# Kernel tuning notes

Hardware: AMD Instinct MI355X
Metric: run time of the kernel (lower is better)

Reference implementation:

```python
import jax, jax.numpy as jnp
import numpy as np

N_ETYPES = 6
N_STEPS = 5
N_ITERS = 6
N_LSTM_LAYERS = 3
NODES_PER_GRAPH = 200


def _uinit(key, shape, fan_in):
    s = 1.0 / np.sqrt(fan_in)
    return jax.random.uniform(key, shape, jnp.float32, -s, s)


def setup_inputs() -> dict:
    key = jax.random.key(0)
    ks = jax.random.split(key, 24)
    N, D = 64000, 64
    G = N // NODES_PER_GRAPH  # 320 graphs
    E = N * 16  # 1,024,000 edges
    feats = jax.random.normal(ks[0], (N, D), jnp.float32)
    # within-graph edges: local endpoint + graph offset
    graph_of_edge = jnp.repeat(jnp.arange(G, dtype=jnp.int32), E // G)
    src = jax.random.randint(ks[1], (E,), 0, NODES_PER_GRAPH, jnp.int32) + graph_of_edge * NODES_PER_GRAPH
    dst = jax.random.randint(ks[2], (E,), 0, NODES_PER_GRAPH, jnp.int32) + graph_of_edge * NODES_PER_GRAPH
    etypes = jax.random.randint(ks[3], (E,), 0, N_ETYPES, jnp.int32)
    node_graph = jnp.repeat(jnp.arange(G, dtype=jnp.int32), NODES_PER_GRAPH)
    # GatedGraphConv params: per-etype Linear(D,D) + GRUCell(D,D) (torch gate order r,z,n)
    W_edge = _uinit(ks[4], (N_ETYPES, D, D), D)
    b_edge = _uinit(ks[5], (N_ETYPES, D), D)
    gru_W_ih = _uinit(ks[6], (3 * D, D), D)
    gru_W_hh = _uinit(ks[7], (3 * D, D), D)
    gru_b_ih = _uinit(ks[8], (3 * D,), D)
    gru_b_hh = _uinit(ks[9], (3 * D,), D)
    # Set2Set LSTM: 3 layers, input 2D (layer0) / D (layers 1,2), hidden D; torch gate order i,f,g,o
    lstm_W_ih0 = _uinit(ks[10], (4 * D, 2 * D), D)
    lstm_W_hh0 = _uinit(ks[11], (4 * D, D), D)
    lstm_b_ih0 = _uinit(ks[12], (4 * D,), D)
    lstm_b_hh0 = _uinit(ks[13], (4 * D,), D)
    lstm_W_ih1 = _uinit(ks[14], (4 * D, D), D)
    lstm_W_hh1 = _uinit(ks[15], (4 * D, D), D)
    lstm_b_ih1 = _uinit(ks[16], (4 * D,), D)
    lstm_b_hh1 = _uinit(ks[17], (4 * D,), D)
    lstm_W_ih2 = _uinit(ks[18], (4 * D, D), D)
    lstm_W_hh2 = _uinit(ks[19], (4 * D, D), D)
    lstm_b_ih2 = _uinit(ks[20], (4 * D,), D)
    lstm_b_hh2 = _uinit(ks[21], (4 * D,), D)
    Wp = _uinit(ks[22], (3, 2 * D), 2 * D)
    bp = _uinit(ks[23], (3,), 2 * D)
    return dict(feats=feats, W_edge=W_edge, b_edge=b_edge,
                gru_W_ih=gru_W_ih, gru_W_hh=gru_W_hh, gru_b_ih=gru_b_ih, gru_b_hh=gru_b_hh,
                lstm_W_ih0=lstm_W_ih0, lstm_W_hh0=lstm_W_hh0, lstm_b_ih0=lstm_b_ih0, lstm_b_hh0=lstm_b_hh0,
                lstm_W_ih1=lstm_W_ih1, lstm_W_hh1=lstm_W_hh1, lstm_b_ih1=lstm_b_ih1, lstm_b_hh1=lstm_b_hh1,
                lstm_W_ih2=lstm_W_ih2, lstm_W_hh2=lstm_W_hh2, lstm_b_ih2=lstm_b_ih2, lstm_b_hh2=lstm_b_hh2,
                Wp=Wp, bp=bp, src=src, dst=dst, etypes=etypes, node_graph=node_graph)


def _ggnn_forward(feats, W_edge, b_edge, gru_W_ih, gru_W_hh, gru_b_ih, gru_b_hh,
                  lstm_params, Wp, bp, src, dst, etypes, node_graph):
    N, D = feats.shape
    G = N // NODES_PER_GRAPH
    h = feats
    # --- GatedGraphConv: 5 steps of etype-typed transform + scatter-sum + GRU ---
    for _ in range(N_STEPS):
        # transform every node by every etype weight (cheap: N << E), then gather per edge
        Wh = jnp.einsum('nd,tdo->tno', h, W_edge) + b_edge[:, None, :]  # [T,N,D]
        msg = Wh[etypes, src]                                           # [E,D] gather
        a = jax.ops.segment_sum(msg, dst, num_segments=N)               # [N,D] scatter-add
        gi = a @ gru_W_ih.T + gru_b_ih
        gh = h @ gru_W_hh.T + gru_b_hh
        i_r, i_z, i_n = jnp.split(gi, 3, -1)
        h_r, h_z, h_n = jnp.split(gh, 3, -1)
        r = jax.nn.sigmoid(i_r + h_r)
        z = jax.nn.sigmoid(i_z + h_z)
        n = jnp.tanh(i_n + r * h_n)
        h = (1.0 - z) * n + z * h
    feat = h
    # --- Set2Set readout ---
    q_star = jnp.zeros((G, 2 * D), feat.dtype)
    hs = jnp.zeros((N_LSTM_LAYERS, G, D), feat.dtype)
    cs = jnp.zeros((N_LSTM_LAYERS, G, D), feat.dtype)
    for _ in range(N_ITERS):
        x = q_star
        new_h, new_c = [], []
        for l, (Wi, Whh, bi, bh) in enumerate(lstm_params):
            gates = x @ Wi.T + bi + hs[l] @ Whh.T + bh
            ii, ff, gg, oo = jnp.split(gates, 4, -1)
            c = jax.nn.sigmoid(ff) * cs[l] + jax.nn.sigmoid(ii) * jnp.tanh(gg)
            x = jax.nn.sigmoid(oo) * jnp.tanh(c)
            new_h.append(x)
            new_c.append(c)
        hs = jnp.stack(new_h)
        cs = jnp.stack(new_c)
        q = x  # [G,D]
        e = jnp.sum(feat * q[node_graph], axis=-1)                         # [N]
        emax = jax.ops.segment_max(e, node_graph, num_segments=G)
        ex = jnp.exp(e - emax[node_graph])
        denom = jax.ops.segment_sum(ex, node_graph, num_segments=G)
        alpha = ex / denom[node_graph]                                     # segment softmax
        readout = jax.ops.segment_sum(feat * alpha[:, None], node_graph, num_segments=G)
        q_star = jnp.concatenate([q, readout], axis=-1)
    return q_star @ Wp.T + bp  # [G,3]


def reference(feats, W_edge, b_edge, gru_W_ih, gru_W_hh, gru_b_ih, gru_b_hh,
              lstm_W_ih0, lstm_W_hh0, lstm_b_ih0, lstm_b_hh0,
              lstm_W_ih1, lstm_W_hh1, lstm_b_ih1, lstm_b_hh1,
              lstm_W_ih2, lstm_W_hh2, lstm_b_ih2, lstm_b_hh2,
              Wp, bp, src, dst, etypes, node_graph):
    lstm_params = [
        (lstm_W_ih0, lstm_W_hh0, lstm_b_ih0, lstm_b_hh0),
        (lstm_W_ih1, lstm_W_hh1, lstm_b_ih1, lstm_b_hh1),
        (lstm_W_ih2, lstm_W_hh2, lstm_b_ih2, lstm_b_hh2),
    ]
    return _ggnn_forward(feats, W_edge, b_edge, gru_W_ih, gru_W_hh, gru_b_ih, gru_b_hh,
                         lstm_params, Wp, bp, src, dst, etypes, node_graph)
```

## Files before the change

kernel.cpp:

```cpp
#include <hip/hip_runtime.h>

typedef unsigned short u16;
typedef unsigned int u32;

#define DIM 64
#define NGRAPH 320
#define NPG 200
#define EPG 3200
#define NSTEPS 5
#define NITERS 6
#define NTILES 13
#define NPAD 208
#define NTHR 1024

typedef __attribute__((ext_vector_type(8))) short bf16x8;
typedef __attribute__((ext_vector_type(4))) float f32x4;

__device__ __forceinline__ float bf2f(u16 u) {
  u32 x = ((u32)u) << 16;
  float f;
  __builtin_memcpy(&f, &x, 4);
  return f;
}
__device__ __forceinline__ u16 f2bf(float f) {
  u32 x;
  __builtin_memcpy(&x, &f, 4);
  x = (x + 0x7FFFu + ((x >> 16) & 1u)) >> 16;
  return (u16)x;
}
__device__ __forceinline__ float bflo(u32 w) {
  u32 x = w << 16;
  float f;
  __builtin_memcpy(&f, &x, 4);
  return f;
}
__device__ __forceinline__ float bfhi(u32 w) {
  u32 x = w & 0xffff0000u;
  float f;
  __builtin_memcpy(&f, &x, 4);
  return f;
}
__device__ __forceinline__ float sigmf(float x) { return 1.0f / (1.0f + __expf(-x)); }
__device__ __forceinline__ int swz(int row, int col) { return row * 64 + (col ^ ((row & 7) << 3)); }


__global__ void __launch_bounds__(256) k_csr(const int* __restrict__ src,
                                             const int* __restrict__ dst,
                                             const int* __restrict__ ety,
                                             u16* __restrict__ recs,
                                             int* __restrict__ rows) {
  __shared__ int cnt[3 * NPG];
  __shared__ int rofs[3 * (NPG + 1)];
  int g = blockIdx.x, tid = threadIdx.x;
  int base = g * NPG;
  for (int i = tid; i < 3 * NPG; i += 256) cnt[i] = 0;
  __syncthreads();
  for (int e = tid; e < EPG; e += 256) {
    int d = dst[g * EPG + e] - base;
    int t = ety[g * EPG + e];
    atomicAdd(&cnt[(t >> 1) * NPG + d], 1);
  }
  __syncthreads();
  if (tid == 0) {
    int s = 0;
    for (int p = 0; p < 3; p++) {
      for (int n = 0; n < NPG; n++) {
        rofs[p * (NPG + 1) + n] = s;
        s += cnt[p * NPG + n];
      }
      rofs[p * (NPG + 1) + NPG] = s;
    }
  }
  __syncthreads();
  for (int i = tid; i < 3 * NPG; i += 256) cnt[i] = rofs[(i / NPG) * (NPG + 1) + (i % NPG)];
  __syncthreads();
  for (int e = tid; e < EPG; e += 256) {
    int d = dst[g * EPG + e] - base;
    int t = ety[g * EPG + e];
    int sl = src[g * EPG + e] - base;
    int pos = atomicAdd(&cnt[(t >> 1) * NPG + d], 1);
    recs[g * EPG + pos] = (u16)((t & 1) * NPG + sl);
  }
  for (int i = tid; i < 3 * (NPG + 1); i += 256) rows[g * 3 * (NPG + 1) + i] = rofs[i];
}

__global__ void __launch_bounds__(256) k_prep(
    const float* __restrict__ W_edge, const float* __restrict__ gWih, const float* __restrict__ gWhh,
    const float* __restrict__ lWi0, const float* __restrict__ lWh0,
    const float* __restrict__ lWi1, const float* __restrict__ lWh1,
    const float* __restrict__ lWi2, const float* __restrict__ lWh2,
    u16* __restrict__ WeTb, u16* __restrict__ Wihb, u16* __restrict__ Whhb,
    u16* __restrict__ WTih0b, u16* __restrict__ WThh0b,
    u16* __restrict__ WTih1b, u16* __restrict__ WThh1b,
    u16* __restrict__ WTih2b, u16* __restrict__ WThh2b) {
  int i = blockIdx.x * 256 + threadIdx.x;
  if (i < 24576) {
    int t = i >> 12, rem = i & 4095, o = rem >> 6, k = rem & 63;
    WeTb[i] = f2bf(W_edge[t * 4096 + k * 64 + o]);
  } else if (i < 36864) {
    int idx = i - 24576;
    Wihb[idx] = f2bf(gWih[idx]);
  } else if (i < 49152) {
    int idx = i - 36864;
    Whhb[idx] = f2bf(gWhh[idx]);
  } else if (i < 81920) {
    int idx = i - 49152;
    int k = idx >> 8, jj = idx & 255;
    WTih0b[idx] = f2bf(lWi0[jj * 128 + k]);
  } else {
    int idx = i - 81920;
    int seg = idx >> 14;
    int r = idx & 16383;
    int k = r >> 8, jj = r & 255;
    const float* sp = seg == 0 ? lWh0 : seg == 1 ? lWi1 : seg == 2 ? lWh1 : seg == 3 ? lWi2 : lWh2;
    u16* dp = seg == 0 ? WThh0b : seg == 1 ? WTih1b : seg == 2 ? WThh1b : seg == 3 ? WTih2b : WThh2b;
    dp[r] = f2bf(sp[jj * 64 + k]);
  }
}


__global__ void __launch_bounds__(NTHR, 4) k_ggnn(
    const float* __restrict__ feats,
    const u16* __restrict__ WeTb, const float* __restrict__ b_edge,
    const u16* __restrict__ Wihb, const u16* __restrict__ Whhb,
    const float* __restrict__ gbih, const float* __restrict__ gbhh,
    const u16* __restrict__ recs, const int* __restrict__ rows,
    const u16* __restrict__ WTih0b, const u16* __restrict__ WThh0b,
    const u16* __restrict__ WTih1b, const u16* __restrict__ WThh1b,
    const u16* __restrict__ WTih2b, const u16* __restrict__ WThh2b,
    const float* __restrict__ b_ih0, const float* __restrict__ b_hh0,
    const float* __restrict__ b_ih1, const float* __restrict__ b_hh1,
    const float* __restrict__ b_ih2, const float* __restrict__ b_hh2,
    const float* __restrict__ Wp, const float* __restrict__ bp,
    float* __restrict__ out) {
  __shared__ __align__(16) u16 hb_s[NPAD * 64];
  __shared__ __align__(16) u16 wh_s[2 * NPG * 64];
  __shared__ __align__(16) float acc_s[NPG * 64];
  __shared__ __align__(16) u16 rec_s[EPG];
  __shared__ int rows_s[3 * (NPG + 1)];
  __shared__ float qstar[128], xbuf[64], hs_s[3][64], cs_s[3][64];
  __shared__ float gates[256], gpart[4 * 256], e_s[NPG], red[16][64], scal[2];

  int g = blockIdx.x, tid = threadIdx.x;
  int lane = tid & 63, wid = tid >> 6;
  int m = lane & 15, quad = lane >> 4;
  int half = lane >> 5, l32 = lane & 31;

  const float* fg = feats + (size_t)g * (NPG * 64);
  for (int i = tid; i < NPG * 64; i += NTHR) hb_s[swz(i >> 6, i & 63)] = f2bf(fg[i]);
  for (int i = tid; i < (NPAD - NPG) * 64; i += NTHR) hb_s[NPG * 64 + i] = 0;
  {
    const u32* r32 = (const u32*)(recs + (size_t)g * EPG);
    u32* rl = (u32*)rec_s;
    for (int i = tid; i < EPG / 2; i += NTHR) rl[i] = r32[i];
  }
  for (int i = tid; i < 3 * (NPG + 1); i += NTHR) rows_s[i] = rows[g * 3 * (NPG + 1) + i];

  float hreg[4][4] = {};
  if (wid < NTILES) {
#pragma unroll
    for (int r = 0; r < 4; r++) {
      int node = wid * 16 + quad * 4 + r;
      if (node < NPG) {
#pragma unroll
        for (int dq = 0; dq < 4; dq++) hreg[r][dq] = fg[node * 64 + dq * 16 + m];
      }
    }
  }

  u16* ab_s = wh_s;
  int ot = wid & 3, hh = wid >> 2;

#pragma unroll 1
  for (int step = 0; step < NSTEPS; step++) {
    __syncthreads();
    {
      float4* z4 = (float4*)acc_s;
      float4 z = {0.f, 0.f, 0.f, 0.f};
      for (int i = tid; i < NPG * 16; i += NTHR) z4[i] = z;
    }
#pragma unroll 1
    for (int ph = 0; ph < 3; ph++) {
      if (ph > 0) __syncthreads();
      {
        const u16* bp0 = WeTb + (((2 * ph) * 64 + ot * 16 + m) * 64) + quad * 8;
        const u16* bp1 = WeTb + (((2 * ph + 1) * 64 + ot * 16 + m) * 64) + quad * 8;
        bf16x8 B00 = *(const bf16x8*)bp0;
        bf16x8 B01 = *(const bf16x8*)(bp0 + 32);
        bf16x8 B10 = *(const bf16x8*)bp1;
        bf16x8 B11 = *(const bf16x8*)(bp1 + 32);
        float bias0 = b_edge[(2 * ph) * 64 + ot * 16 + m];
        float bias1 = b_edge[(2 * ph + 1) * 64 + ot * 16 + m];
        for (int nt = hh; nt < NTILES; nt += 4) {
          int arow = nt * 16 + m;
          bf16x8 a0 = *(const bf16x8*)(hb_s + swz(arow, quad * 8));
          bf16x8 a1 = *(const bf16x8*)(hb_s + swz(arow, quad * 8 + 32));
          f32x4 c = {0.f, 0.f, 0.f, 0.f};
          c = __builtin_amdgcn_mfma_f32_16x16x32_bf16(a0, B00, c, 0, 0, 0);
          c = __builtin_amdgcn_mfma_f32_16x16x32_bf16(a1, B01, c, 0, 0, 0);
#pragma unroll
          for (int r = 0; r < 4; r++) {
            int node = nt * 16 + quad * 4 + r;
            if (node < NPG) wh_s[node * 64 + ot * 16 + m] = f2bf(c[r] + bias0);
          }
        }
        for (int nt = 3 - hh; nt < NTILES; nt += 4) {
          int arow = nt * 16 + m;
          bf16x8 a0 = *(const bf16x8*)(hb_s + swz(arow, quad * 8));
          bf16x8 a1 = *(const bf16x8*)(hb_s + swz(arow, quad * 8 + 32));
          f32x4 c = {0.f, 0.f, 0.f, 0.f};
          c = __builtin_amdgcn_mfma_f32_16x16x32_bf16(a0, B10, c, 0, 0, 0);
          c = __builtin_amdgcn_mfma_f32_16x16x32_bf16(a1, B11, c, 0, 0, 0);
#pragma unroll
          for (int r = 0; r < 4; r++) {
            int node = nt * 16 + quad * 4 + r;
            if (node < NPG) wh_s[(NPG + node) * 64 + ot * 16 + m] = f2bf(c[r] + bias1);
          }
        }
      }
      __syncthreads();
      const int* rowp = rows_s + ph * (NPG + 1);
      for (int q = 0; q < 13; q++) {
        int n = q * 16 + wid;
        if (n >= NPG) continue;
        int rs = rowp[n], re = rowp[n + 1];
        float r0 = 0.f, r1 = 0.f;
        int e = rs;
        for (; e + 4 <= re; e += 4) {
          int pA = rec_s[e + half];
          int pB = rec_s[e + 2 + half];
          u32 wA = *(const u32*)(wh_s + pA * 64 + 2 * l32);
          u32 wB = *(const u32*)(wh_s + pB * 64 + 2 * l32);
          r0 += bflo(wA) + bflo(wB);
          r1 += bfhi(wA) + bfhi(wB);
        }
        if (e + 2 <= re) {
          int pA = rec_s[e + half];
          u32 wA = *(const u32*)(wh_s + pA * 64 + 2 * l32);
          r0 += bflo(wA);
          r1 += bfhi(wA);
          e += 2;
        }
        if (e < re && half == 0) {
          int pA = rec_s[e];
          u32 wA = *(const u32*)(wh_s + pA * 64 + 2 * l32);
          r0 += bflo(wA);
          r1 += bfhi(wA);
        }
        r0 += __shfl_xor(r0, 32);
        r1 += __shfl_xor(r1, 32);
        if (lane < 32) {
          float2* p = (float2*)(acc_s + n * 64 + 2 * l32);
          float2 v = *p;
          v.x += r0;
          v.y += r1;
          *p = v;
        }
      }
    }
    __syncthreads();
    for (int idx = tid; idx < NPG * 32; idx += NTHR) {
      int n = idx >> 5, jj = idx & 31;
      float2 v = *(const float2*)(acc_s + n * 64 + 2 * jj);
      u32 pk = (u32)f2bf(v.x) | ((u32)f2bf(v.y) << 16);
      *(u32*)(ab_s + n * 64 + ((2 * jj) ^ ((n & 7) << 3))) = pk;
    }
    __syncthreads();
    if (wid < NTILES) {
      int nt = wid;
      int arow = nt * 16 + m;
      bf16x8 aa0 = *(const bf16x8*)(ab_s + swz(arow, quad * 8));
      bf16x8 aa1 = *(const bf16x8*)(ab_s + swz(arow, quad * 8 + 32));
      bf16x8 ah0 = *(const bf16x8*)(hb_s + swz(arow, quad * 8));
      bf16x8 ah1 = *(const bf16x8*)(hb_s + swz(arow, quad * 8 + 32));
#pragma unroll
      for (int dq = 0; dq < 4; dq++) {
        int d = dq * 16 + m;
        f32x4 z4 = {0.f, 0.f, 0.f, 0.f};
        const u16* bi = Wihb + (dq * 16 + m) * 64 + quad * 8;
        const u16* bh = Whhb + (dq * 16 + m) * 64 + quad * 8;
        f32x4 cr = z4;
        {
          bf16x8 b0 = *(const bf16x8*)bi, b1 = *(const bf16x8*)(bi + 32);
          bf16x8 c0 = *(const bf16x8*)bh, c1 = *(const bf16x8*)(bh + 32);
          cr = __builtin_amdgcn_mfma_f32_16x16x32_bf16(ah0, c0, cr, 0, 0, 0);
          cr = __builtin_amdgcn_mfma_f32_16x16x32_bf16(ah1, c1, cr, 0, 0, 0);
          cr = __builtin_amdgcn_mfma_f32_16x16x32_bf16(aa0, b0, cr, 0, 0, 0);
          cr = __builtin_amdgcn_mfma_f32_16x16x32_bf16(aa1, b1, cr, 0, 0, 0);
        }
        const u16* bi2 = Wihb + ((4 + dq) * 16 + m) * 64 + quad * 8;
        const u16* bh2 = Whhb + ((4 + dq) * 16 + m) * 64 + quad * 8;
        f32x4 cz = z4;
        {
          bf16x8 b0 = *(const bf16x8*)bi2, b1 = *(const bf16x8*)(bi2 + 32);
          bf16x8 c0 = *(const bf16x8*)bh2, c1 = *(const bf16x8*)(bh2 + 32);
          cz = __builtin_amdgcn_mfma_f32_16x16x32_bf16(ah0, c0, cz, 0, 0, 0);
          cz = __builtin_amdgcn_mfma_f32_16x16x32_bf16(ah1, c1, cz, 0, 0, 0);
          cz = __builtin_amdgcn_mfma_f32_16x16x32_bf16(aa0, b0, cz, 0, 0, 0);
          cz = __builtin_amdgcn_mfma_f32_16x16x32_bf16(aa1, b1, cz, 0, 0, 0);
        }
        const u16* bi3 = Wihb + ((8 + dq) * 16 + m) * 64 + quad * 8;
        const u16* bh3 = Whhb + ((8 + dq) * 16 + m) * 64 + quad * 8;
        f32x4 ci = z4, ch = z4;
        {
          bf16x8 b0 = *(const bf16x8*)bi3, b1 = *(const bf16x8*)(bi3 + 32);
          bf16x8 c0 = *(const bf16x8*)bh3, c1 = *(const bf16x8*)(bh3 + 32);
          ci = __builtin_amdgcn_mfma_f32_16x16x32_bf16(aa0, b0, ci, 0, 0, 0);
          ci = __builtin_amdgcn_mfma_f32_16x16x32_bf16(aa1, b1, ci, 0, 0, 0);
          ch = __builtin_amdgcn_mfma_f32_16x16x32_bf16(ah0, c0, ch, 0, 0, 0);
          ch = __builtin_amdgcn_mfma_f32_16x16x32_bf16(ah1, c1, ch, 0, 0, 0);
        }
        float bi_r = gbih[d], bh_r = gbhh[d];
        float bi_z = gbih[64 + d], bh_z = gbhh[64 + d];
        float bi_n = gbih[128 + d], bh_n = gbhh[128 + d];
#pragma unroll
        for (int r = 0; r < 4; r++) {
          int node = nt * 16 + quad * 4 + r;
          if (node < NPG) {
            float rr = sigmf(cr[r] + bi_r + bh_r);
            float zz = sigmf(cz[r] + bi_z + bh_z);
            float nn = tanhf(ci[r] + bi_n + rr * (ch[r] + bh_n));
            float hv = hreg[r][dq];
            float hnew = (1.0f - zz) * nn + zz * hv;
            hreg[r][dq] = hnew;
            hb_s[swz(node, d)] = f2bf(hnew);
            if (step == NSTEPS - 1) acc_s[node * 64 + d] = hnew;
          }
        }
      }
    }
  }
  __syncthreads();
  const float* feat_s = acc_s;

  int j = tid & 255, part = tid >> 8;
  float bs0 = 0.f, bs1 = 0.f, bs2 = 0.f;
  if (tid < 256) {
    bs0 = b_ih0[tid] + b_hh0[tid];
    bs1 = b_ih1[tid] + b_hh1[tid];
    bs2 = b_ih2[tid] + b_hh2[tid];
  }
  if (tid < 128) qstar[tid] = 0.f;
  if (tid < 64) {
    xbuf[tid] = 0.f;
    for (int l = 0; l < 3; l++) {
      hs_s[l][tid] = 0.f;
      cs_s[l][tid] = 0.f;
    }
  }
  __syncthreads();
#pragma unroll 1
  for (int it = 0; it < NITERS; it++) {
    {
      float a0 = 0.f;
      if (part == 0) {
#pragma unroll 8
        for (int k = 0; k < 48; k++) a0 += qstar[k] * bf2f(WTih0b[k * 256 + j]);
      } else if (part == 1) {
#pragma unroll 8
        for (int k = 48; k < 96; k++) a0 += qstar[k] * bf2f(WTih0b[k * 256 + j]);
      } else if (part == 2) {
#pragma unroll 8
        for (int k = 96; k < 128; k++) a0 += qstar[k] * bf2f(WTih0b[k * 256 + j]);
#pragma unroll 8
        for (int k = 0; k < 16; k++) a0 += hs_s[0][k] * bf2f(WThh0b[k * 256 + j]);
      } else {
#pragma unroll 8
        for (int k = 16; k < 64; k++) a0 += hs_s[0][k] * bf2f(WThh0b[k * 256 + j]);
      }
      gpart[part * 256 + j] = a0;
    }
    __syncthreads();
    if (tid < 256)
      gates[tid] = gpart[tid] + gpart[256 + tid] + gpart[512 + tid] + gpart[768 + tid] + bs0;
    __syncthreads();
    if (tid < 64) {
      float cc = sigmf(gates[64 + tid]) * cs_s[0][tid] + sigmf(gates[tid]) * tanhf(gates[128 + tid]);
      float x = sigmf(gates[192 + tid]) * tanhf(cc);
      cs_s[0][tid] = cc;
      hs_s[0][tid] = x;
      xbuf[tid] = x;
    }
    __syncthreads();
#pragma unroll 1
    for (int l = 1; l < 3; l++) {
      const u16* W = (l == 1) ? ((part < 2) ? WTih1b : WThh1b)
                              : ((part < 2) ? WTih2b : WThh2b);
      const float* xv = (part < 2) ? xbuf : hs_s[l];
      int k0 = (part & 1) * 32;
      float a0 = 0.f;
#pragma unroll 8
      for (int k = k0; k < k0 + 32; k++) a0 += xv[k] * bf2f(W[k * 256 + j]);
      gpart[part * 256 + j] = a0;
      __syncthreads();
      float bsl = (l == 1) ? bs1 : bs2;
      if (tid < 256)
        gates[tid] = gpart[tid] + gpart[256 + tid] + gpart[512 + tid] + gpart[768 + tid] + bsl;
      __syncthreads();
      if (tid < 64) {
        float cc = sigmf(gates[64 + tid]) * cs_s[l][tid] + sigmf(gates[tid]) * tanhf(gates[128 + tid]);
        float x = sigmf(gates[192 + tid]) * tanhf(cc);
        cs_s[l][tid] = cc;
        hs_s[l][tid] = x;
        xbuf[tid] = x;
      }
      __syncthreads();
    }
    for (int n = wid; n < NPG; n += 16) {
      float v = feat_s[n * 64 + lane] * xbuf[lane];
      for (int off = 32; off > 0; off >>= 1) v += __shfl_down(v, off);
      if (lane == 0) e_s[n] = v;
    }
    __syncthreads();
    if (tid < 64) {
      float mx = -1e30f;
      for (int n = lane; n < NPG; n += 64) mx = fmaxf(mx, e_s[n]);
      for (int off = 32; off > 0; off >>= 1) mx = fmaxf(mx, __shfl_down(mx, off));
      mx = __shfl(mx, 0);
      float ssum = 0.f;
      for (int n = lane; n < NPG; n += 64) {
        float ex = __expf(e_s[n] - mx);
        e_s[n] = ex;
        ssum += ex;
      }
      for (int off = 32; off > 0; off >>= 1) ssum += __shfl_down(ssum, off);
      if (lane == 0) scal[0] = ssum;
    }
    __syncthreads();
    float denom = scal[0];
    {
      float r = 0.f;
      for (int n = wid; n < NPG; n += 16) r += feat_s[n * 64 + lane] * e_s[n];
      red[wid][lane] = r;
    }
    __syncthreads();
    if (tid < 64) {
      float ro = 0.f;
#pragma unroll
      for (int ww = 0; ww < 16; ww++) ro += red[ww][lane];
      qstar[lane] = xbuf[lane];
      qstar[64 + lane] = ro / denom;
    }
    __syncthreads();
  }
  if (tid < 3) {
    float s = bp[tid];
    for (int k = 0; k < 128; k++) s += qstar[k] * Wp[tid * 128 + k];
    out[g * 3 + tid] = s;
  }
}


extern "C" void kernel_launch(void* const* d_in, const int* in_sizes, int n_in,
                              void* d_out, int out_size, void* d_ws, size_t ws_size,
                              hipStream_t stream) {
  const float* feats  = (const float*)d_in[0];
  const float* W_edge = (const float*)d_in[1];
  const float* b_edge = (const float*)d_in[2];
  const float* gWih   = (const float*)d_in[3];
  const float* gWhh   = (const float*)d_in[4];
  const float* gbih   = (const float*)d_in[5];
  const float* gbhh   = (const float*)d_in[6];
  const float* lWi0   = (const float*)d_in[7];
  const float* lWh0   = (const float*)d_in[8];
  const float* lbi0   = (const float*)d_in[9];
  const float* lbh0   = (const float*)d_in[10];
  const float* lWi1   = (const float*)d_in[11];
  const float* lWh1   = (const float*)d_in[12];
  const float* lbi1   = (const float*)d_in[13];
  const float* lbh1   = (const float*)d_in[14];
  const float* lWi2   = (const float*)d_in[15];
  const float* lWh2   = (const float*)d_in[16];
  const float* lbi2   = (const float*)d_in[17];
  const float* lbh2   = (const float*)d_in[18];
  const float* Wp     = (const float*)d_in[19];
  const float* bp     = (const float*)d_in[20];
  const int* src      = (const int*)d_in[21];
  const int* dst      = (const int*)d_in[22];
  const int* ety      = (const int*)d_in[23];
  float* out = (float*)d_out;

  char* ws = (char*)d_ws;
  u16* recs    = (u16*)ws;
  int* rows    = (int*)(ws + 2048000);
  u16* WeTb    = (u16*)(ws + 2819840);
  u16* Wihb    = (u16*)(ws + 2868992);
  u16* Whhb    = (u16*)(ws + 2893568);
  u16* WTih0b  = (u16*)(ws + 2918144);
  u16* WThh0b  = (u16*)(ws + 2983680);
  u16* WTih1b  = (u16*)(ws + 3016448);
  u16* WThh1b  = (u16*)(ws + 3049216);
  u16* WTih2b  = (u16*)(ws + 3081984);
  u16* WThh2b  = (u16*)(ws + 3114752);

  k_csr<<<NGRAPH, 256, 0, stream>>>(src, dst, ety, recs, rows);
  k_prep<<<640, 256, 0, stream>>>(W_edge, gWih, gWhh, lWi0, lWh0, lWi1, lWh1, lWi2, lWh2,
                                  WeTb, Wihb, Whhb, WTih0b, WThh0b, WTih1b, WThh1b, WTih2b, WThh2b);
  k_ggnn<<<NGRAPH, NTHR, 0, stream>>>(feats, WeTb, b_edge, Wihb, Whhb, gbih, gbhh, recs, rows,
                                      WTih0b, WThh0b, WTih1b, WThh1b, WTih2b, WThh2b,
                                      lbi0, lbh0, lbi1, lbh1, lbi2, lbh2, Wp, bp, out);
}
```

Baseline: 808.7 us.

## Halve block size, keep gather accumulators in registers, shrink shared memory

The fused GGNN kernel now runs 512 threads per graph instead of 1024. The edge CSR is split into six per-etype partitions so each message phase transforms only one etype into a single shared buffer. Per-node aggregation sums are held in 50 unrolled registers per thread rather than a float accumulator array in shared memory, and the final node features go to a global scratch buffer. The shared footprint shrinks and small buffers are aliased into one union, aiming for more resident blocks per CU and less LDS traffic, in exchange for more barriers per step (six phases instead of three), higher register pressure, and global reads during the Set2Set readout.

```diff
diff --git a/kernel.cpp b/kernel.cpp
--- a/kernel.cpp
+++ b/kernel.cpp
@@ -11,7 +11,7 @@
 #define NITERS 6
 #define NTILES 13
 #define NPAD 208
-#define NTHR 1024
+#define NTHR 512
 
 typedef __attribute__((ext_vector_type(8))) short bf16x8;
 typedef __attribute__((ext_vector_type(4))) float f32x4;
@@ -43,27 +43,30 @@
 __device__ __forceinline__ float sigmf(float x) { return 1.0f / (1.0f + __expf(-x)); }
 __device__ __forceinline__ int swz(int row, int col) { return row * 64 + (col ^ ((row & 7) << 3)); }
 
+#define REP25(M) M(0) M(1) M(2) M(3) M(4) M(5) M(6) M(7) M(8) M(9) M(10) M(11) M(12) \
+                 M(13) M(14) M(15) M(16) M(17) M(18) M(19) M(20) M(21) M(22) M(23) M(24)
+
 
 __global__ void __launch_bounds__(256) k_csr(const int* __restrict__ src,
                                              const int* __restrict__ dst,
                                              const int* __restrict__ ety,
                                              u16* __restrict__ recs,
                                              int* __restrict__ rows) {
-  __shared__ int cnt[3 * NPG];
-  __shared__ int rofs[3 * (NPG + 1)];
+  __shared__ int cnt[6 * NPG];
+  __shared__ int rofs[6 * (NPG + 1)];
   int g = blockIdx.x, tid = threadIdx.x;
   int base = g * NPG;
-  for (int i = tid; i < 3 * NPG; i += 256) cnt[i] = 0;
+  for (int i = tid; i < 6 * NPG; i += 256) cnt[i] = 0;
   __syncthreads();
   for (int e = tid; e < EPG; e += 256) {
     int d = dst[g * EPG + e] - base;
     int t = ety[g * EPG + e];
-    atomicAdd(&cnt[(t >> 1) * NPG + d], 1);
+    atomicAdd(&cnt[t * NPG + d], 1);
   }
   __syncthreads();
   if (tid == 0) {
     int s = 0;
-    for (int p = 0; p < 3; p++) {
+    for (int p = 0; p < 6; p++) {
       for (int n = 0; n < NPG; n++) {
         rofs[p * (NPG + 1) + n] = s;
         s += cnt[p * NPG + n];
@@ -72,16 +75,16 @@
     }
   }
   __syncthreads();
-  for (int i = tid; i < 3 * NPG; i += 256) cnt[i] = rofs[(i / NPG) * (NPG + 1) + (i % NPG)];
+  for (int i = tid; i < 6 * NPG; i += 256) cnt[i] = rofs[(i / NPG) * (NPG + 1) + (i % NPG)];
   __syncthreads();
   for (int e = tid; e < EPG; e += 256) {
     int d = dst[g * EPG + e] - base;
     int t = ety[g * EPG + e];
     int sl = src[g * EPG + e] - base;
-    int pos = atomicAdd(&cnt[(t >> 1) * NPG + d], 1);
-    recs[g * EPG + pos] = (u16)((t & 1) * NPG + sl);
-  }
-  for (int i = tid; i < 3 * (NPG + 1); i += 256) rows[g * 3 * (NPG + 1) + i] = rofs[i];
+    int pos = atomicAdd(&cnt[t * NPG + d], 1);
+    recs[g * EPG + pos] = (u16)sl;
+  }
+  for (int i = tid; i < 6 * (NPG + 1); i += 256) rows[g * 6 * (NPG + 1) + i] = rofs[i];
 }
 
 __global__ void __launch_bounds__(256) k_prep(
@@ -132,14 +135,22 @@
     const float* __restrict__ b_ih1, const float* __restrict__ b_hh1,
     const float* __restrict__ b_ih2, const float* __restrict__ b_hh2,
     const float* __restrict__ Wp, const float* __restrict__ bp,
-    float* __restrict__ out) {
+    float* __restrict__ featg, float* __restrict__ out) {
   __shared__ __align__(16) u16 hb_s[NPAD * 64];
-  __shared__ __align__(16) u16 wh_s[2 * NPG * 64];
-  __shared__ __align__(16) float acc_s[NPG * 64];
-  __shared__ __align__(16) u16 rec_s[EPG];
-  __shared__ int rows_s[3 * (NPG + 1)];
-  __shared__ float qstar[128], xbuf[64], hs_s[3][64], cs_s[3][64];
-  __shared__ float gates[256], gpart[4 * 256], e_s[NPG], red[16][64], scal[2];
+  __shared__ __align__(16) u16 whab[NPG * 64];
+  __shared__ __align__(16) char u_s[11232];
+
+  u16* rec_s = (u16*)u_s;
+  int* rows_s = (int*)(u_s + 6400);
+  float* qstar = (float*)u_s;
+  float* xbuf = (float*)(u_s + 512);
+  float* hs_f = (float*)(u_s + 768);
+  float* cs_f = (float*)(u_s + 1536);
+  float* gates = (float*)(u_s + 2304);
+  float* gpart = (float*)(u_s + 3328);
+  float* e_s = (float*)(u_s + 5376);
+  float* red_f = (float*)(u_s + 6176);
+  float* scal = (float*)(u_s + 8224);
 
   int g = blockIdx.x, tid = threadIdx.x;
   int lane = tid & 63, wid = tid >> 6;
@@ -147,6 +158,7 @@
   int half = lane >> 5, l32 = lane & 31;
 
   const float* fg = feats + (size_t)g * (NPG * 64);
+  float* fo = featg + (size_t)g * (NPG * 64);
   for (int i = tid; i < NPG * 64; i += NTHR) hb_s[swz(i >> 6, i & 63)] = f2bf(fg[i]);
   for (int i = tid; i < (NPAD - NPG) * 64; i += NTHR) hb_s[NPG * 64 + i] = 0;
   {
@@ -154,120 +166,107 @@
     u32* rl = (u32*)rec_s;
     for (int i = tid; i < EPG / 2; i += NTHR) rl[i] = r32[i];
   }
-  for (int i = tid; i < 3 * (NPG + 1); i += NTHR) rows_s[i] = rows[g * 3 * (NPG + 1) + i];
-
-  float hreg[4][4] = {};
-  if (wid < NTILES) {
-#pragma unroll
-    for (int r = 0; r < 4; r++) {
-      int node = wid * 16 + quad * 4 + r;
-      if (node < NPG) {
-#pragma unroll
-        for (int dq = 0; dq < 4; dq++) hreg[r][dq] = fg[node * 64 + dq * 16 + m];
-      }
-    }
-  }
-
-  u16* ab_s = wh_s;
-  int ot = wid & 3, hh = wid >> 2;
+  for (int i = tid; i < 6 * (NPG + 1); i += NTHR) rows_s[i] = rows[g * 6 * (NPG + 1) + i];
+
+  float hreg[2][4][4] = {};
+#pragma unroll
+  for (int ti = 0; ti < 2; ti++) {
+    int nt = wid + 8 * ti;
+    if (nt < NTILES) {
+#pragma unroll
+      for (int r = 0; r < 4; r++) {
+        int node = nt * 16 + quad * 4 + r;
+        if (node < NPG) {
+#pragma unroll
+          for (int dq = 0; dq < 4; dq++) hreg[ti][r][dq] = fg[node * 64 + dq * 16 + m];
+        }
+      }
+    }
+  }
+
+  u16* ab_s = whab;
+  int ot = wid & 3;
+
+#define ACC_DECL(q) float a0_##q, a1_##q;
+  REP25(ACC_DECL)
+#define ACC_ZERO(q) a0_##q = 0.f; a1_##q = 0.f;
+#define GATHER(q)                                                  \
+  {                                                                \
+    int n = (q)*8 + wid;                                           \
+    int rs = rowp[n], re = rowp[n + 1];                            \
+    float r0 = 0.f, r1 = 0.f;                                      \
+    int e = rs;                                                    \
+    for (; e + 4 <= re; e += 4) {                                  \
+      int pA = rec_s[e + half];                                    \
+      int pB = rec_s[e + 2 + half];                                \
+      u32 wA = *(const u32*)(whab + pA * 64 + 2 * l32);            \
+      u32 wB = *(const u32*)(whab + pB * 64 + 2 * l32);            \
+      r0 += bflo(wA) + bflo(wB);                                   \
+      r1 += bfhi(wA) + bfhi(wB);                                   \
+    }                                                              \
+    if (e + 2 <= re) {                                             \
+      int pA = rec_s[e + half];                                    \
+      u32 wA = *(const u32*)(whab + pA * 64 + 2 * l32);            \
+      r0 += bflo(wA);                                              \
+      r1 += bfhi(wA);                                              \
+      e += 2;                                                      \
+    }                                                              \
+    if (e < re && half == 0) {                                     \
+      int pA = rec_s[e];                                           \
+      u32 wA = *(const u32*)(whab + pA * 64 + 2 * l32);            \
+      r0 += bflo(wA);                                              \
+      r1 += bfhi(wA);                                              \
+    }                                                              \
+    a0_##q += r0;                                                  \
+    a1_##q += r1;                                                  \
+  }
+#define FLUSH(q)                                                   \
+  {                                                                \
+    float s0 = a0_##q + __shfl_xor(a0_##q, 32);                    \
+    float s1 = a1_##q + __shfl_xor(a1_##q, 32);                    \
+    if (lane < 32) {                                               \
+      int n = (q)*8 + wid;                                         \
+      u32 pk = (u32)f2bf(s0) | ((u32)f2bf(s1) << 16);              \
+      *(u32*)(ab_s + n * 64 + ((2 * l32) ^ ((n & 7) << 3))) = pk;  \
+    }                                                              \
+  }
 
 #pragma unroll 1
   for (int step = 0; step < NSTEPS; step++) {
-    __syncthreads();
-    {
-      float4* z4 = (float4*)acc_s;
-      float4 z = {0.f, 0.f, 0.f, 0.f};
-      for (int i = tid; i < NPG * 16; i += NTHR) z4[i] = z;
-    }
+    REP25(ACC_ZERO)
 #pragma unroll 1
-    for (int ph = 0; ph < 3; ph++) {
-      if (ph > 0) __syncthreads();
+    for (int t = 0; t < 6; t++) {
+      __syncthreads();
       {
-        const u16* bp0 = WeTb + (((2 * ph) * 64 + ot * 16 + m) * 64) + quad * 8;
-        const u16* bp1 = WeTb + (((2 * ph + 1) * 64 + ot * 16 + m) * 64) + quad * 8;
-        bf16x8 B00 = *(const bf16x8*)bp0;
-        bf16x8 B01 = *(const bf16x8*)(bp0 + 32);
-        bf16x8 B10 = *(const bf16x8*)bp1;
-        bf16x8 B11 = *(const bf16x8*)(bp1 + 32);
-        float bias0 = b_edge[(2 * ph) * 64 + ot * 16 + m];
-        float bias1 = b_edge[(2 * ph + 1) * 64 + ot * 16 + m];
-        for (int nt = hh; nt < NTILES; nt += 4) {
+        const u16* bpt = WeTb + ((t * 64 + ot * 16 + m) * 64) + quad * 8;
+        bf16x8 B0 = *(const bf16x8*)bpt;
+        bf16x8 B1 = *(const bf16x8*)(bpt + 32);
+        float bias = b_edge[t * 64 + ot * 16 + m];
+        for (int nt = (wid >> 2); nt < NTILES; nt += 2) {
           int arow = nt * 16 + m;
           bf16x8 a0 = *(const bf16x8*)(hb_s + swz(arow, quad * 8));
           bf16x8 a1 = *(const bf16x8*)(hb_s + swz(arow, quad * 8 + 32));
           f32x4 c = {0.f, 0.f, 0.f, 0.f};
-          c = __builtin_amdgcn_mfma_f32_16x16x32_bf16(a0, B00, c, 0, 0, 0);
-          c = __builtin_amdgcn_mfma_f32_16x16x32_bf16(a1, B01, c, 0, 0, 0);
+          c = __builtin_amdgcn_mfma_f32_16x16x32_bf16(a0, B0, c, 0, 0, 0);
+          c = __builtin_amdgcn_mfma_f32_16x16x32_bf16(a1, B1, c, 0, 0, 0);
 #pragma unroll
           for (int r = 0; r < 4; r++) {
             int node = nt * 16 + quad * 4 + r;
-            if (node < NPG) wh_s[node * 64 + ot * 16 + m] = f2bf(c[r] + bias0);
+            if (node < NPG) whab[node * 64 + ot * 16 + m] = f2bf(c[r] + bias);
           }
         }
-        for (int nt = 3 - hh; nt < NTILES; nt += 4) {
-          int arow = nt * 16 + m;
-          bf16x8 a0 = *(const bf16x8*)(hb_s + swz(arow, quad * 8));
-          bf16x8 a1 = *(const bf16x8*)(hb_s + swz(arow, quad * 8 + 32));
-          f32x4 c = {0.f, 0.f, 0.f, 0.f};
-          c = __builtin_amdgcn_mfma_f32_16x16x32_bf16(a0, B10, c, 0, 0, 0);
-          c = __builtin_amdgcn_mfma_f32_16x16x32_bf16(a1, B11, c, 0, 0, 0);
-#pragma unroll
-          for (int r = 0; r < 4; r++) {
-            int node = nt * 16 + quad * 4 + r;
-            if (node < NPG) wh_s[(NPG + node) * 64 + ot * 16 + m] = f2bf(c[r] + bias1);
-          }
-        }
       }
       __syncthreads();
-      const int* rowp = rows_s + ph * (NPG + 1);
-      for (int q = 0; q < 13; q++) {
-        int n = q * 16 + wid;
-        if (n >= NPG) continue;
-        int rs = rowp[n], re = rowp[n + 1];
-        float r0 = 0.f, r1 = 0.f;
-        int e = rs;
-        for (; e + 4 <= re; e += 4) {
-          int pA = rec_s[e + half];
-          int pB = rec_s[e + 2 + half];
-          u32 wA = *(const u32*)(wh_s + pA * 64 + 2 * l32);
-          u32 wB = *(const u32*)(wh_s + pB * 64 + 2 * l32);
-          r0 += bflo(wA) + bflo(wB);
-          r1 += bfhi(wA) + bfhi(wB);
-        }
-        if (e + 2 <= re) {
-          int pA = rec_s[e + half];
-          u32 wA = *(const u32*)(wh_s + pA * 64 + 2 * l32);
-          r0 += bflo(wA);
-          r1 += bfhi(wA);
-          e += 2;
-        }
-        if (e < re && half == 0) {
-          int pA = rec_s[e];
-          u32 wA = *(const u32*)(wh_s + pA * 64 + 2 * l32);
-          r0 += bflo(wA);
-          r1 += bfhi(wA);
-        }
-        r0 += __shfl_xor(r0, 32);
-        r1 += __shfl_xor(r1, 32);
-        if (lane < 32) {
-          float2* p = (float2*)(acc_s + n * 64 + 2 * l32);
-          float2 v = *p;
-          v.x += r0;
-          v.y += r1;
-          *p = v;
-        }
-      }
-    }
-    __syncthreads();
-    for (int idx = tid; idx < NPG * 32; idx += NTHR) {
-      int n = idx >> 5, jj = idx & 31;
-      float2 v = *(const float2*)(acc_s + n * 64 + 2 * jj);
-      u32 pk = (u32)f2bf(v.x) | ((u32)f2bf(v.y) << 16);
-      *(u32*)(ab_s + n * 64 + ((2 * jj) ^ ((n & 7) << 3))) = pk;
-    }
-    __syncthreads();
-    if (wid < NTILES) {
-      int nt = wid;
+      const int* rowp = rows_s + t * (NPG + 1);
+      REP25(GATHER)
+    }
+    __syncthreads();
+    REP25(FLUSH)
+    __syncthreads();
+#pragma unroll
+    for (int ti = 0; ti < 2; ti++) {
+      int nt = wid + 8 * ti;
+      if (nt >= NTILES) continue;
       int arow = nt * 16 + m;
       bf16x8 aa0 = *(const bf16x8*)(ab_s + swz(arow, quad * 8));
       bf16x8 aa1 = *(const bf16x8*)(ab_s + swz(arow, quad * 8 + 32));
@@ -320,18 +319,18 @@
             float rr = sigmf(cr[r] + bi_r + bh_r);
             float zz = sigmf(cz[r] + bi_z + bh_z);
             float nn = tanhf(ci[r] + bi_n + rr * (ch[r] + bh_n));
-            float hv = hreg[r][dq];
+            float hv = hreg[ti][r][dq];
             float hnew = (1.0f - zz) * nn + zz * hv;
-            hreg[r][dq] = hnew;
+            hreg[ti][r][dq] = hnew;
             hb_s[swz(node, d)] = f2bf(hnew);
-            if (step == NSTEPS - 1) acc_s[node * 64 + d] = hnew;
+            if (step == NSTEPS - 1) fo[node * 64 + d] = hnew;
           }
         }
       }
     }
   }
-  __syncthreads();
-  const float* feat_s = acc_s;
+  __threadfence_block();
+  __syncthreads();
 
   int j = tid & 255, part = tid >> 8;
   float bs0 = 0.f, bs1 = 0.f, bs2 = 0.f;
@@ -344,8 +343,8 @@
   if (tid < 64) {
     xbuf[tid] = 0.f;
     for (int l = 0; l < 3; l++) {
-      hs_s[l][tid] = 0.f;
-      cs_s[l][tid] = 0.f;
+      hs_f[l * 64 + tid] = 0.f;
+      cs_f[l * 64 + tid] = 0.f;
     }
   }
   __syncthreads();
@@ -355,59 +354,50 @@
       float a0 = 0.f;
       if (part == 0) {
 #pragma unroll 8
-        for (int k = 0; k < 48; k++) a0 += qstar[k] * bf2f(WTih0b[k * 256 + j]);
-      } else if (part == 1) {
-#pragma unroll 8
-        for (int k = 48; k < 96; k++) a0 += qstar[k] * bf2f(WTih0b[k * 256 + j]);
-      } else if (part == 2) {
+        for (int k = 0; k < 96; k++) a0 += qstar[k] * bf2f(WTih0b[k * 256 + j]);
+      } else {
 #pragma unroll 8
         for (int k = 96; k < 128; k++) a0 += qstar[k] * bf2f(WTih0b[k * 256 + j]);
 #pragma unroll 8
-        for (int k = 0; k < 16; k++) a0 += hs_s[0][k] * bf2f(WThh0b[k * 256 + j]);
-      } else {
-#pragma unroll 8
-        for (int k = 16; k < 64; k++) a0 += hs_s[0][k] * bf2f(WThh0b[k * 256 + j]);
+        for (int k = 0; k < 64; k++) a0 += hs_f[k] * bf2f(WThh0b[k * 256 + j]);
       }
       gpart[part * 256 + j] = a0;
     }
     __syncthreads();
-    if (tid < 256)
-      gates[tid] = gpart[tid] + gpart[256 + tid] + gpart[512 + tid] + gpart[768 + tid] + bs0;
+    if (tid < 256) gates[tid] = gpart[tid] + gpart[256 + tid] + bs0;
     __syncthreads();
     if (tid < 64) {
-      float cc = sigmf(gates[64 + tid]) * cs_s[0][tid] + sigmf(gates[tid]) * tanhf(gates[128 + tid]);
+      float cc = sigmf(gates[64 + tid]) * cs_f[tid] + sigmf(gates[tid]) * tanhf(gates[128 + tid]);
       float x = sigmf(gates[192 + tid]) * tanhf(cc);
-      cs_s[0][tid] = cc;
-      hs_s[0][tid] = x;
+      cs_f[tid] = cc;
+      hs_f[tid] = x;
       xbuf[tid] = x;
     }
     __syncthreads();
 #pragma unroll 1
     for (int l = 1; l < 3; l++) {
-      const u16* W = (l == 1) ? ((part < 2) ? WTih1b : WThh1b)
-                              : ((part < 2) ? WTih2b : WThh2b);
-      const float* xv = (part < 2) ? xbuf : hs_s[l];
-      int k0 = (part & 1) * 32;
+      const u16* W = (l == 1) ? (part ? WThh1b : WTih1b) : (part ? WThh2b : WTih2b);
+      const float* xv = part ? (hs_f + l * 64) : xbuf;
       float a0 = 0.f;
 #pragma unroll 8
-      for (int k = k0; k < k0 + 32; k++) a0 += xv[k] * bf2f(W[k * 256 + j]);
+      for (int k = 0; k < 64; k++) a0 += xv[k] * bf2f(W[k * 256 + j]);
       gpart[part * 256 + j] = a0;
       __syncthreads();
       float bsl = (l == 1) ? bs1 : bs2;
-      if (tid < 256)
-        gates[tid] = gpart[tid] + gpart[256 + tid] + gpart[512 + tid] + gpart[768 + tid] + bsl;
+      if (tid < 256) gates[tid] = gpart[tid] + gpart[256 + tid] + bsl;
       __syncthreads();
       if (tid < 64) {
-        float cc = sigmf(gates[64 + tid]) * cs_s[l][tid] + sigmf(gates[tid]) * tanhf(gates[128 + tid]);
+        float cc = sigmf(gates[64 + tid]) * cs_f[l * 64 + tid] +
+                   sigmf(gates[tid]) * tanhf(gates[128 + tid]);
         float x = sigmf(gates[192 + tid]) * tanhf(cc);
-        cs_s[l][tid] = cc;
-        hs_s[l][tid] = x;
+        cs_f[l * 64 + tid] = cc;
+        hs_f[l * 64 + tid] = x;
         xbuf[tid] = x;
       }
       __syncthreads();
     }
-    for (int n = wid; n < NPG; n += 16) {
-      float v = feat_s[n * 64 + lane] * xbuf[lane];
+    for (int n = wid; n < NPG; n += 8) {
+      float v = fo[n * 64 + lane] * xbuf[lane];
       for (int off = 32; off > 0; off >>= 1) v += __shfl_down(v, off);
       if (lane == 0) e_s[n] = v;
     }
@@ -430,14 +420,14 @@
     float denom = scal[0];
     {
       float r = 0.f;
-      for (int n = wid; n < NPG; n += 16) r += feat_s[n * 64 + lane] * e_s[n];
-      red[wid][lane] = r;
+      for (int n = wid; n < NPG; n += 8) r += fo[n * 64 + lane] * e_s[n];
+      red_f[wid * 64 + lane] = r;
     }
     __syncthreads();
     if (tid < 64) {
       float ro = 0.f;
 #pragma unroll
-      for (int ww = 0; ww < 16; ww++) ro += red[ww][lane];
+      for (int ww = 0; ww < 8; ww++) ro += red_f[ww * 64 + lane];
       qstar[lane] = xbuf[lane];
       qstar[64 + lane] = ro / denom;
     }
@@ -483,20 +473,21 @@
   char* ws = (char*)d_ws;
   u16* recs    = (u16*)ws;
   int* rows    = (int*)(ws + 2048000);
-  u16* WeTb    = (u16*)(ws + 2819840);
-  u16* Wihb    = (u16*)(ws + 2868992);
-  u16* Whhb    = (u16*)(ws + 2893568);
-  u16* WTih0b  = (u16*)(ws + 2918144);
-  u16* WThh0b  = (u16*)(ws + 2983680);
-  u16* WTih1b  = (u16*)(ws + 3016448);
-  u16* WThh1b  = (u16*)(ws + 3049216);
-  u16* WTih2b  = (u16*)(ws + 3081984);
-  u16* WThh2b  = (u16*)(ws + 3114752);
+  u16* WeTb    = (u16*)(ws + 3591680);
+  u16* Wihb    = (u16*)(ws + 3640832);
+  u16* Whhb    = (u16*)(ws + 3665408);
+  u16* WTih0b  = (u16*)(ws + 3689984);
+  u16* WThh0b  = (u16*)(ws + 3755520);
+  u16* WTih1b  = (u16*)(ws + 3788288);
+  u16* WThh1b  = (u16*)(ws + 3821056);
+  u16* WTih2b  = (u16*)(ws + 3853824);
+  u16* WThh2b  = (u16*)(ws + 3886592);
+  float* featg = (float*)(ws + 3919360);
 
   k_csr<<<NGRAPH, 256, 0, stream>>>(src, dst, ety, recs, rows);
   k_prep<<<640, 256, 0, stream>>>(W_edge, gWih, gWhh, lWi0, lWh0, lWi1, lWh1, lWi2, lWh2,
                                   WeTb, Wihb, Whhb, WTih0b, WThh0b, WTih1b, WThh1b, WTih2b, WThh2b);
   k_ggnn<<<NGRAPH, NTHR, 0, stream>>>(feats, WeTb, b_edge, Wihb, Whhb, gbih, gbhh, recs, rows,
                                       WTih0b, WThh0b, WTih1b, WThh1b, WTih2b, WThh2b,
-                                      lbi0, lbh0, lbi1, lbh1, lbi2, lbh2, Wp, bp, out);
-}
+                                      lbi0, lbh0, lbi1, lbh1, lbi2, lbh2, Wp, bp, featg, out);
+}
```

New measurement: 814.2 us. About the same (+0.7%).
